# Kernel tuning notes

Measured on AMD Instinct MI355X. Metric: run time of the kernel, lower is better.

Reference implementation:

```python
import jax, jax.numpy as jnp
import numpy as np

B, N, M, H, NH = 128, 4096, 64, 512, 4
IN, OUT = 256, 256
NH2 = 2 * NH  # read/write heads interleaved: even idx = read, odd idx = write
EPS = 1e-8


def setup_inputs() -> dict:
    key = jax.random.key(0)
    ks = jax.random.split(key, 20)
    nrm = lambda k, shape, s=0.05: (jax.random.normal(k, shape, jnp.float32) * s)
    return {
        'in_data': jax.random.normal(ks[0], (B, IN), jnp.float32),
        'memory': jax.random.normal(ks[1], (B, N, M), jnp.float32) * 0.1,
        'h_prev': jax.random.normal(ks[2], (B, H), jnp.float32),
        'c_prev': jax.random.normal(ks[3], (B, H), jnp.float32),
        'prev_reads': jax.random.normal(ks[4], (NH, B, M), jnp.float32),
        'prev_weights': jax.random.uniform(ks[5], (NH2, B, N), jnp.float32),
        # controller LSTMCell (input = in_data ++ prev_reads)
        'W_ih': nrm(ks[6], (4 * H, IN + NH * M)),
        'b_ih': jnp.zeros((4 * H,), jnp.float32),
        'W_hh': nrm(ks[7], (4 * H, H)),
        'b_hh': jnp.zeros((4 * H,), jnp.float32),
        # output layer over [h ++ reads]
        'W_out': nrm(ks[8], (OUT, H + NH * M)),
        'b_out': jnp.zeros((OUT,), jnp.float32),
        # per-head addressing params, stacked over the 2*NH heads (fed with c-state)
        'Wk': nrm(ks[9], (NH2, M, H)), 'bk': jnp.zeros((NH2, M), jnp.float32),
        'Wbeta': nrm(ks[10], (NH2, H)), 'bbeta': jnp.zeros((NH2,), jnp.float32),
        'Wg': nrm(ks[11], (NH2, H)), 'bg': jnp.zeros((NH2,), jnp.float32),
        'Ws': nrm(ks[12], (NH2, 3, H)), 'bs': jnp.zeros((NH2, 3), jnp.float32),
        'Wgam': nrm(ks[13], (NH2, H)), 'bgam': jnp.zeros((NH2,), jnp.float32),
        'We': nrm(ks[14], (NH2, M, H)), 'be': jnp.zeros((NH2, M), jnp.float32),
        'Wa': nrm(ks[15], (NH2, M, H)), 'ba': jnp.zeros((NH2, M), jnp.float32),
    }


def reference(in_data, memory, h_prev, c_prev, prev_reads, prev_weights,
              W_ih, b_ih, W_hh, b_hh, W_out, b_out,
              Wk, bk, Wbeta, bbeta, Wg, bg, Ws, bs, Wgam, bgam, We, be, Wa, ba):
    bsz = in_data.shape[0]
    # controller LSTM step on [x ++ prev_reads]
    x = jnp.concatenate([in_data, jnp.swapaxes(prev_reads, 0, 1).reshape(bsz, -1)], axis=-1)
    gates = x @ W_ih.T + h_prev @ W_hh.T + b_ih + b_hh
    gi, gf, gg, go = jnp.split(gates, 4, axis=-1)
    c = jax.nn.sigmoid(gf) * c_prev + jax.nn.sigmoid(gi) * jnp.tanh(gg)
    h = jax.nn.sigmoid(go) * jnp.tanh(c)  # |h| < 1, so clamp(-20, 20) is identity

    mem = memory
    reads = []
    for i in range(NH2):  # fixed small loop; even = read head, odd = write head
        keyv = c @ Wk[i].T + bk[i]                                    # [B, M]
        beta = jax.nn.softplus(c @ Wbeta[i] + bbeta[i])[:, None]      # [B, 1]
        g = jax.nn.sigmoid(c @ Wg[i] + bg[i])[:, None]                # [B, 1]
        s = jax.nn.softmax(c @ Ws[i].T + bs[i], axis=-1)              # [B, 3]
        gamma = 1.0 + jax.nn.softplus(c @ Wgam[i] + bgam[i])[:, None]  # [B, 1]
        # content addressing: cosine similarity, sharpened softmax
        sim = jnp.einsum('bnm,bm->bn', mem, keyv)
        sim = sim / (jnp.linalg.norm(mem, axis=-1) * jnp.linalg.norm(keyv, axis=-1, keepdims=True) + EPS)
        wc = jax.nn.softmax(beta * sim, axis=-1)
        # interpolate, circular shift (-1, 0, +1), sharpen
        wg_ = g * wc + (1.0 - g) * prev_weights[i]
        wsft = (s[:, 0:1] * jnp.roll(wg_, -1, axis=1)
                + s[:, 1:2] * wg_
                + s[:, 2:3] * jnp.roll(wg_, 1, axis=1))
        wpow = wsft ** gamma
        w = wpow / (jnp.sum(wpow, axis=1, keepdims=True) + EPS)
        if i % 2 == 0:
            reads.append(jnp.einsum('bn,bnm->bm', w, mem))
        else:
            e = jax.nn.sigmoid(c @ We[i].T + be[i])                   # erase [B, M]
            a = jnp.tanh(c @ Wa[i].T + ba[i])                         # add   [B, M]
            mem = mem * (1.0 - w[:, :, None] * e[:, None, :]) + w[:, :, None] * a[:, None, :]

    out = jax.nn.sigmoid(jnp.concatenate([h] + reads, axis=-1) @ W_out.T + b_out)
    return out
```

## Files before the change

kernel.cpp:

```cpp
#include <hip/hip_runtime.h>
#include <math.h>

#define BSZ 128
#define NN_ 4096
#define MM_ 64
#define HH_ 512
#define EPSF 1e-8f

__device__ __forceinline__ float sigmoidf_(float x) { return 1.0f / (1.0f + expf(-x)); }
__device__ __forceinline__ float softplusf_(float x) { return fmaxf(x, 0.0f) + log1pf(expf(-fabsf(x))); }

__global__ __launch_bounds__(256) void k_gemm_gates(const float* __restrict__ in_data,
                                                    const float* __restrict__ prev_reads,
                                                    const float* __restrict__ h_prev,
                                                    const float* __restrict__ W_ih,
                                                    const float* __restrict__ W_hh,
                                                    float* __restrict__ Cp) {
    __shared__ float Alds[64 * 65];
    __shared__ float Wlds[64 * 65];
    int t = threadIdx.x;
    int n0 = blockIdx.x * 64;
    int b0 = blockIdx.y * 64;
    float* C = Cp + (size_t)blockIdx.z * (BSZ * 2048);
    int ob = (t & 15) * 4;
    int bb = (t >> 4) * 4;
    float acc[4][4];
#pragma unroll
    for (int i = 0; i < 4; ++i)
#pragma unroll
        for (int j = 0; j < 4; ++j) acc[i][j] = 0.f;
    for (int kt = 0; kt < 4; ++kt) {
        int k0 = blockIdx.z * 256 + kt * 64;
        __syncthreads();
        for (int i = 0; i < 4; ++i) {
            int f = t + 256 * i;
            int row = f >> 4, kk = (f & 15) * 4;
            int k = k0 + kk;
            float4 v;
            if (k < 256) v = *(const float4*)(in_data + ((b0 + row) << 8) + k);
            else if (k < 512) {
                int q = k - 256;
                v = *(const float4*)(prev_reads + (((q >> 6) * BSZ + b0 + row) << 6) + (q & 63));
            } else v = *(const float4*)(h_prev + ((b0 + row) << 9) + (k - 512));
            Alds[(kk + 0) * 65 + row] = v.x;
            Alds[(kk + 1) * 65 + row] = v.y;
            Alds[(kk + 2) * 65 + row] = v.z;
            Alds[(kk + 3) * 65 + row] = v.w;
        }
        for (int i = 0; i < 4; ++i) {
            int f = t + 256 * i;
            int o = f >> 4, kk = (f & 15) * 4;
            int j = n0 + o, k = k0 + kk;
            const float* src = (k < 512) ? (W_ih + (size_t)j * 512 + k)
                                         : (W_hh + (size_t)j * 512 + (k - 512));
            float4 v = *(const float4*)src;
            Wlds[(kk + 0) * 65 + o] = v.x;
            Wlds[(kk + 1) * 65 + o] = v.y;
            Wlds[(kk + 2) * 65 + o] = v.z;
            Wlds[(kk + 3) * 65 + o] = v.w;
        }
        __syncthreads();
        for (int kk = 0; kk < 64; ++kk) {
            const float* wp = &Wlds[kk * 65 + ob];
            const float* ap = &Alds[kk * 65 + bb];
            float w0 = wp[0], w1 = wp[1], w2 = wp[2], w3 = wp[3];
#pragma unroll
            for (int j = 0; j < 4; ++j) {
                float av = ap[j];
                acc[0][j] = fmaf(w0, av, acc[0][j]);
                acc[1][j] = fmaf(w1, av, acc[1][j]);
                acc[2][j] = fmaf(w2, av, acc[2][j]);
                acc[3][j] = fmaf(w3, av, acc[3][j]);
            }
        }
    }
#pragma unroll
    for (int i = 0; i < 4; ++i)
#pragma unroll
        for (int j = 0; j < 4; ++j)
            C[(size_t)(b0 + bb + j) * 2048 + n0 + ob + i] = acc[i][j];
}

__global__ void k_lstm(const float* __restrict__ gatesP, const float* __restrict__ b_ih,
                       const float* __restrict__ b_hh, const float* __restrict__ c_prev,
                       float* __restrict__ cbuf, float* __restrict__ hbuf) {
    int idx = blockIdx.x * blockDim.x + threadIdx.x;
    if (idx >= BSZ * HH_) return;
    int b = idx >> 9, j = idx & 511;
    float gi = b_ih[j]        + b_hh[j];
    float gf = b_ih[512 + j]  + b_hh[512 + j];
    float gg = b_ih[1024 + j] + b_hh[1024 + j];
    float go = b_ih[1536 + j] + b_hh[1536 + j];
#pragma unroll
    for (int p = 0; p < 4; ++p) {
        const float* gr = gatesP + (size_t)p * (BSZ * 2048) + (size_t)b * 2048;
        gi += gr[j];
        gf += gr[512 + j];
        gg += gr[1024 + j];
        go += gr[1536 + j];
    }
    float cc = sigmoidf_(gf) * c_prev[idx] + sigmoidf_(gi) * tanhf(gg);
    float hh = sigmoidf_(go) * tanhf(cc);
    cbuf[idx] = cc;
    hbuf[idx] = hh;
}

__device__ __forceinline__ const float* whead_row_ptr(const float* Wk, const float* Wbeta,
                                                      const float* Wg, const float* Ws,
                                                      const float* Wgam, const float* We,
                                                      const float* Wa, int r) {
    int i = r / 198, q = r - i * 198;
    if (q < 64)  return Wk + (size_t)((i << 6) + q) * 512;
    if (q == 64) return Wbeta + (size_t)i * 512;
    if (q == 65) return Wg + (size_t)i * 512;
    if (q <= 68) return Ws + (size_t)(i * 3 + q - 66) * 512;
    if (q == 69) return Wgam + (size_t)i * 512;
    if (q < 134) return We + (size_t)((i << 6) + q - 70) * 512;
    return Wa + (size_t)((i << 6) + q - 134) * 512;
}

__global__ __launch_bounds__(256) void k_gemm_head(const float* __restrict__ A,
                                                   const float* __restrict__ Wk,
                                                   const float* __restrict__ Wbeta,
                                                   const float* __restrict__ Wg,
                                                   const float* __restrict__ Ws,
                                                   const float* __restrict__ Wgam,
                                                   const float* __restrict__ We,
                                                   const float* __restrict__ Wa,
                                                   float* __restrict__ Cp) {
    __shared__ float Alds[64 * 65];
    __shared__ float Wlds[64 * 65];
    int t = threadIdx.x;
    int n0 = blockIdx.x * 64;
    int b0 = blockIdx.y * 64;
    float* C = Cp + (size_t)blockIdx.z * (BSZ * 1408);
    int ob = (t & 15) * 4;
    int bb = (t >> 4) * 4;
    float acc[4][4];
#pragma unroll
    for (int i = 0; i < 4; ++i)
#pragma unroll
        for (int j = 0; j < 4; ++j) acc[i][j] = 0.f;
    for (int kt = 0; kt < 4; ++kt) {
        int k0 = blockIdx.z * 256 + kt * 64;
        __syncthreads();
        for (int i = 0; i < 4; ++i) {
            int f = t + 256 * i;
            int row = f >> 4, kk = (f & 15) * 4;
            float4 v = *(const float4*)(A + (size_t)(b0 + row) * 512 + k0 + kk);
            Alds[(kk + 0) * 65 + row] = v.x;
            Alds[(kk + 1) * 65 + row] = v.y;
            Alds[(kk + 2) * 65 + row] = v.z;
            Alds[(kk + 3) * 65 + row] = v.w;
        }
        for (int i = 0; i < 4; ++i) {
            int f = t + 256 * i;
            int o = f >> 4, kk = (f & 15) * 4;
            int r = n0 + o;
            float4 v = make_float4(0.f, 0.f, 0.f, 0.f);
            if (r < 1386) {
                const float* p = whead_row_ptr(Wk, Wbeta, Wg, Ws, Wgam, We, Wa, r) + k0 + kk;
                v = *(const float4*)p;
            }
            Wlds[(kk + 0) * 65 + o] = v.x;
            Wlds[(kk + 1) * 65 + o] = v.y;
            Wlds[(kk + 2) * 65 + o] = v.z;
            Wlds[(kk + 3) * 65 + o] = v.w;
        }
        __syncthreads();
        for (int kk = 0; kk < 64; ++kk) {
            const float* wp = &Wlds[kk * 65 + ob];
            const float* ap = &Alds[kk * 65 + bb];
            float w0 = wp[0], w1 = wp[1], w2 = wp[2], w3 = wp[3];
#pragma unroll
            for (int j = 0; j < 4; ++j) {
                float av = ap[j];
                acc[0][j] = fmaf(w0, av, acc[0][j]);
                acc[1][j] = fmaf(w1, av, acc[1][j]);
                acc[2][j] = fmaf(w2, av, acc[2][j]);
                acc[3][j] = fmaf(w3, av, acc[3][j]);
            }
        }
    }
#pragma unroll
    for (int i = 0; i < 4; ++i)
#pragma unroll
        for (int j = 0; j < 4; ++j)
            C[(size_t)(b0 + bb + j) * 1408 + n0 + ob + i] = acc[i][j];
}

__global__ __launch_bounds__(256) void k_headact(const float* __restrict__ C0,
                                                 const float* __restrict__ C1,
                                                 const float* __restrict__ bk, const float* __restrict__ bbeta,
                                                 const float* __restrict__ bg, const float* __restrict__ bs,
                                                 const float* __restrict__ bgam, const float* __restrict__ be,
                                                 const float* __restrict__ ba,
                                                 float* __restrict__ keys, float* __restrict__ knorm,
                                                 float* __restrict__ betaA, float* __restrict__ gA,
                                                 float* __restrict__ gammaA, float* __restrict__ sA,
                                                 float* __restrict__ eA, float* __restrict__ aA) {
    __shared__ float sk[64];
    __shared__ float s3[3];
    int blk = blockIdx.x;
    int i = blk >> 7, b = blk & 127;
    int q = threadIdx.x;
    float val = 0.f;
    if (q < 198) {
        float bv = (q < 64)   ? bk[(i << 6) + q]
                 : (q == 64)  ? bbeta[i]
                 : (q == 65)  ? bg[i]
                 : (q <= 68)  ? bs[i * 3 + q - 66]
                 : (q == 69)  ? bgam[i]
                 : (q < 134)  ? be[(i << 6) + q - 70]
                              : ba[(i << 6) + q - 134];
        size_t idx = (size_t)b * 1408 + i * 198 + q;
        val = C0[idx] + C1[idx] + bv;
    }
    if (q < 64) { keys[(size_t)(i * BSZ + b) * 64 + q] = val; sk[q] = val * val; }
    if (q >= 66 && q <= 68) s3[q - 66] = val;
    __syncthreads();
    if (q == 0) {
        float s = 0.f;
        for (int m2 = 0; m2 < 64; ++m2) s += sk[m2];
        knorm[i * BSZ + b] = sqrtf(s);
    }
    if (q == 64) betaA[i * BSZ + b] = softplusf_(val);
    if (q == 65) gA[i * BSZ + b] = sigmoidf_(val);
    if (q == 69) gammaA[i * BSZ + b] = 1.f + softplusf_(val);
    if (q == 66) {
        float mx = fmaxf(s3[0], fmaxf(s3[1], s3[2]));
        float e0 = expf(s3[0] - mx), e1 = expf(s3[1] - mx), e2 = expf(s3[2] - mx);
        float inv = 1.f / (e0 + e1 + e2);
        sA[(i * BSZ + b) * 3 + 0] = e0 * inv;
        sA[(i * BSZ + b) * 3 + 1] = e1 * inv;
        sA[(i * BSZ + b) * 3 + 2] = e2 * inv;
    }
    if (q >= 70 && q < 134)  eA[(size_t)(i * BSZ + b) * 64 + (q - 70)] = sigmoidf_(val);
    if (q >= 134 && q < 198) aA[(size_t)(i * BSZ + b) * 64 + (q - 134)] = tanhf(val);
}

__global__ __launch_bounds__(256) void k_pass2(const float* __restrict__ mem,
                                               const float* __restrict__ wbuf,
                                               const float* __restrict__ eA, const float* __restrict__ aA,
                                               const float* __restrict__ keys, const float* __restrict__ knorm,
                                               float* __restrict__ sims, float* __restrict__ r_out,
                                               int napply, int nsims, int sh0, int sh1,
                                               int read_state, int read_head, int read_idx) {
    __shared__ __align__(16) float rbuf[16][64];
    int t = threadIdx.x;
    int lane = t & 15, grp = t >> 4;
    int base = blockIdx.x * 64;
    int b = base >> 12;
    int m4 = lane * 4;
    float4 e1 = *(const float4*)(eA + (size_t)(1 * BSZ + b) * 64 + m4);
    float4 a1 = *(const float4*)(aA + (size_t)(1 * BSZ + b) * 64 + m4);
    float4 e3 = *(const float4*)(eA + (size_t)(3 * BSZ + b) * 64 + m4);
    float4 a3 = *(const float4*)(aA + (size_t)(3 * BSZ + b) * 64 + m4);
    float4 e5 = *(const float4*)(eA + (size_t)(5 * BSZ + b) * 64 + m4);
    float4 a5 = *(const float4*)(aA + (size_t)(5 * BSZ + b) * 64 + m4);
    float4 k0v = make_float4(0.f, 0.f, 0.f, 0.f), k1v = k0v;
    float kn0v = 0.f, kn1v = 0.f;
    if (nsims > 0) { k0v = *(const float4*)(keys + (size_t)(sh0 * BSZ + b) * 64 + m4); kn0v = knorm[sh0 * BSZ + b]; }
    if (nsims > 1) { k1v = *(const float4*)(keys + (size_t)(sh1 * BSZ + b) * 64 + m4); kn1v = knorm[sh1 * BSZ + b]; }
    const float* w1p = wbuf + (size_t)1 * BSZ * NN_;
    const float* w3p = wbuf + (size_t)3 * BSZ * NN_;
    const float* w5p = wbuf + (size_t)5 * BSZ * NN_;
    const float* wrp = (read_head >= 0) ? (wbuf + (size_t)read_head * BSZ * NN_) : nullptr;
    float* sim0 = sims + (size_t)sh0 * BSZ * NN_;
    float* sim1 = sims + (size_t)sh1 * BSZ * NN_;

    float4 racc = make_float4(0.f, 0.f, 0.f, 0.f);
    for (int it = 0; it < 4; ++it) {
        int row = base + it * 16 + grp;
        float4 m = *(const float4*)(mem + (size_t)row * 64 + m4);
        float4 mr = m;
        if (napply >= 1) {
            float w = w1p[row];
            m.x = m.x * (1.f - w * e1.x) + w * a1.x;
            m.y = m.y * (1.f - w * e1.y) + w * a1.y;
            m.z = m.z * (1.f - w * e1.z) + w * a1.z;
            m.w = m.w * (1.f - w * e1.w) + w * a1.w;
            if (read_state == 1) mr = m;
        }
        if (napply >= 2) {
            float w = w3p[row];
            m.x = m.x * (1.f - w * e3.x) + w * a3.x;
            m.y = m.y * (1.f - w * e3.y) + w * a3.y;
            m.z = m.z * (1.f - w * e3.z) + w * a3.z;
            m.w = m.w * (1.f - w * e3.w) + w * a3.w;
            if (read_state == 2) mr = m;
        }
        if (napply >= 3) {
            float w = w5p[row];
            m.x = m.x * (1.f - w * e5.x) + w * a5.x;
            m.y = m.y * (1.f - w * e5.y) + w * a5.y;
            m.z = m.z * (1.f - w * e5.z) + w * a5.z;
            m.w = m.w * (1.f - w * e5.w) + w * a5.w;
            if (read_state == 3) mr = m;
        }
        if (read_head >= 0) {
            float wr = wrp[row];
            racc.x = fmaf(wr, mr.x, racc.x);
            racc.y = fmaf(wr, mr.y, racc.y);
            racc.z = fmaf(wr, mr.z, racc.z);
            racc.w = fmaf(wr, mr.w, racc.w);
        }
        if (nsims > 0) {
            float d0 = m.x * k0v.x + m.y * k0v.y + m.z * k0v.z + m.w * k0v.w;
            float nn = m.x * m.x + m.y * m.y + m.z * m.z + m.w * m.w;
            float d1 = 0.f;
            if (nsims > 1) d1 = m.x * k1v.x + m.y * k1v.y + m.z * k1v.z + m.w * k1v.w;
#pragma unroll
            for (int off = 8; off >= 1; off >>= 1) {
                d0 += __shfl_xor(d0, off, 16);
                nn += __shfl_xor(nn, off, 16);
                if (nsims > 1) d1 += __shfl_xor(d1, off, 16);
            }
            if (lane == 0) {
                float nm = sqrtf(nn);
                sim0[row] = d0 / (nm * kn0v + EPSF);
                if (nsims > 1) sim1[row] = d1 / (nm * kn1v + EPSF);
            }
        }
    }
    if (read_head >= 0) {
        *(float4*)(&rbuf[grp][m4]) = racc;
        __syncthreads();
        if (t < 64) {
            float s = 0.f;
#pragma unroll
            for (int g2 = 0; g2 < 16; ++g2) s += rbuf[g2][t];
            atomicAdd(&r_out[(size_t)(read_idx * BSZ + b) * 64 + t], s);
        }
    }
}

__global__ __launch_bounds__(1024) void k_weights(const float* __restrict__ sims,
                                                  const float* __restrict__ prev_w,
                                                  const float* __restrict__ betaA, const float* __restrict__ gA,
                                                  const float* __restrict__ gammaA, const float* __restrict__ sA,
                                                  float* __restrict__ wout_base, int head0) {
    __shared__ float wg[NN_];
    __shared__ float redm[16], reds[16], redp[16];
    int h = head0 + blockIdx.y, b = blockIdx.x;
    int hb = h * BSZ + b;
    float beta = betaA[hb], g = gA[hb], gamma = gammaA[hb];
    float s0 = sA[hb * 3 + 0], s1 = sA[hb * 3 + 1], s2 = sA[hb * 3 + 2];
    const float* sim = sims + (size_t)hb * NN_;
    const float* pw = prev_w + (size_t)hb * NN_;
    float* wout = wout_base + (size_t)hb * NN_;
    int t = threadIdx.x, wv = t >> 6, ln = t & 63;
    float tv[4];
    float lmax = -3.4e38f;
#pragma unroll
    for (int j = 0; j < 4; ++j) {
        float x = beta * sim[t + 1024 * j];
        tv[j] = x;
        lmax = fmaxf(lmax, x);
    }
#pragma unroll
    for (int off = 32; off >= 1; off >>= 1) lmax = fmaxf(lmax, __shfl_xor(lmax, off));
    if (ln == 0) redm[wv] = lmax;
    __syncthreads();
    float Mx = redm[0];
#pragma unroll
    for (int k = 1; k < 16; ++k) Mx = fmaxf(Mx, redm[k]);
    float lsum = 0.f;
#pragma unroll
    for (int j = 0; j < 4; ++j) { float ex = expf(tv[j] - Mx); tv[j] = ex; lsum += ex; }
#pragma unroll
    for (int off = 32; off >= 1; off >>= 1) lsum += __shfl_xor(lsum, off);
    if (ln == 0) reds[wv] = lsum;
    __syncthreads();
    float S = 0.f;
#pragma unroll
    for (int k = 0; k < 16; ++k) S += reds[k];
    float invS = 1.f / S;
#pragma unroll
    for (int j = 0; j < 4; ++j) {
        int n = t + 1024 * j;
        wg[n] = g * tv[j] * invS + (1.f - g) * pw[n];
    }
    __syncthreads();
    float lsum2 = 0.f;
#pragma unroll
    for (int j = 0; j < 4; ++j) {
        int n = t + 1024 * j;
        float wsft = s0 * wg[(n + 1) & (NN_ - 1)] + s1 * wg[n] + s2 * wg[(n - 1) & (NN_ - 1)];
        float wp = powf(wsft, gamma);
        tv[j] = wp;
        lsum2 += wp;
    }
#pragma unroll
    for (int off = 32; off >= 1; off >>= 1) lsum2 += __shfl_xor(lsum2, off);
    if (ln == 0) redp[wv] = lsum2;
    __syncthreads();
    float S2 = 0.f;
#pragma unroll
    for (int k = 0; k < 16; ++k) S2 += redp[k];
    float inv2 = 1.f / (S2 + EPSF);
#pragma unroll
    for (int j = 0; j < 4; ++j) wout[t + 1024 * j] = tv[j] * inv2;
}

__global__ __launch_bounds__(256) void k_out_full(const float* __restrict__ hbuf,
                                                  const float* __restrict__ rbuf,
                                                  const float* __restrict__ W_out,
                                                  const float* __restrict__ b_out,
                                                  float* __restrict__ out) {
    __shared__ float Alds[64 * 65];
    __shared__ float Wlds[64 * 65];
    int t = threadIdx.x;
    int n0 = blockIdx.x * 64;
    int b0 = blockIdx.y * 64;
    int ob = (t & 15) * 4;
    int bb = (t >> 4) * 4;
    float acc[4][4];
#pragma unroll
    for (int i = 0; i < 4; ++i)
#pragma unroll
        for (int j = 0; j < 4; ++j) acc[i][j] = 0.f;
    for (int k0 = 0; k0 < 768; k0 += 64) {
        __syncthreads();
        for (int i = 0; i < 4; ++i) {
            int f = t + 256 * i;
            int rb = f >> 4, kk = (f & 15) * 4;
            int k = k0 + kk;
            float4 v;
            if (k < 512) v = *(const float4*)(hbuf + ((b0 + rb) << 9) + k);
            else {
                int q = k - 512;
                v = *(const float4*)(rbuf + (((q >> 6) * BSZ + b0 + rb) << 6) + (q & 63));
            }
            Alds[(kk + 0) * 65 + rb] = v.x;
            Alds[(kk + 1) * 65 + rb] = v.y;
            Alds[(kk + 2) * 65 + rb] = v.z;
            Alds[(kk + 3) * 65 + rb] = v.w;
        }
        for (int i = 0; i < 4; ++i) {
            int f = t + 256 * i;
            int o = f >> 4, kk = (f & 15) * 4;
            float4 v = *(const float4*)(W_out + (size_t)(n0 + o) * 768 + k0 + kk);
            Wlds[(kk + 0) * 65 + o] = v.x;
            Wlds[(kk + 1) * 65 + o] = v.y;
            Wlds[(kk + 2) * 65 + o] = v.z;
            Wlds[(kk + 3) * 65 + o] = v.w;
        }
        __syncthreads();
        for (int kk = 0; kk < 64; ++kk) {
            const float* wp = &Wlds[kk * 65 + ob];
            const float* ap = &Alds[kk * 65 + bb];
            float w0 = wp[0], w1 = wp[1], w2 = wp[2], w3 = wp[3];
#pragma unroll
            for (int j = 0; j < 4; ++j) {
                float av = ap[j];
                acc[0][j] = fmaf(w0, av, acc[0][j]);
                acc[1][j] = fmaf(w1, av, acc[1][j]);
                acc[2][j] = fmaf(w2, av, acc[2][j]);
                acc[3][j] = fmaf(w3, av, acc[3][j]);
            }
        }
    }
#pragma unroll
    for (int i = 0; i < 4; ++i)
#pragma unroll
        for (int j = 0; j < 4; ++j)
            out[(size_t)(b0 + bb + j) * 256 + n0 + ob + i] = sigmoidf_(acc[i][j] + b_out[n0 + ob + i]);
}

extern "C" void kernel_launch(void* const* d_in, const int* in_sizes, int n_in,
                              void* d_out, int out_size, void* d_ws, size_t ws_size,
                              hipStream_t stream) {
    const float* in_data      = (const float*)d_in[0];
    const float* memory       = (const float*)d_in[1];
    const float* h_prev       = (const float*)d_in[2];
    const float* c_prev       = (const float*)d_in[3];
    const float* prev_reads   = (const float*)d_in[4];
    const float* prev_weights = (const float*)d_in[5];
    const float* W_ih = (const float*)d_in[6];
    const float* b_ih = (const float*)d_in[7];
    const float* W_hh = (const float*)d_in[8];
    const float* b_hh = (const float*)d_in[9];
    const float* W_out = (const float*)d_in[10];
    const float* b_out = (const float*)d_in[11];
    const float* Wk   = (const float*)d_in[12];
    const float* bk   = (const float*)d_in[13];
    const float* Wbeta = (const float*)d_in[14];
    const float* bbeta = (const float*)d_in[15];
    const float* Wg   = (const float*)d_in[16];
    const float* bg   = (const float*)d_in[17];
    const float* Ws   = (const float*)d_in[18];
    const float* bs   = (const float*)d_in[19];
    const float* Wgam = (const float*)d_in[20];
    const float* bgam = (const float*)d_in[21];
    const float* We   = (const float*)d_in[22];
    const float* be   = (const float*)d_in[23];
    const float* Wa   = (const float*)d_in[24];
    const float* ba   = (const float*)d_in[25];

    float* ws = (float*)d_ws;
    size_t o_r      = 0;
    size_t zero_floats = 32768;
    size_t o_gatesP = zero_floats;
    size_t o_cheadP = o_gatesP + 1048576;
    size_t o_c     = o_cheadP + 360448;
    size_t o_h     = o_c + 65536;
    size_t o_keys  = o_h + 65536;
    size_t o_knorm = o_keys + 57344;
    size_t o_beta  = o_knorm + 1024;
    size_t o_g     = o_beta + 1024;
    size_t o_gamma = o_g + 1024;
    size_t o_s     = o_gamma + 1024;
    size_t o_e     = o_s + 3072;
    size_t o_a     = o_e + 57344;
    size_t o_sims  = o_a + 57344;
    size_t o_w     = o_sims + 3670016;

    float* rbuf   = ws + o_r;
    float* gatesP = ws + o_gatesP;
    float* CheadP = ws + o_cheadP;
    float* cbuf   = ws + o_c;
    float* hbuf   = ws + o_h;
    float* keys   = ws + o_keys;
    float* knorm  = ws + o_knorm;
    float* betaA  = ws + o_beta;
    float* gA     = ws + o_g;
    float* gammaA = ws + o_gamma;
    float* sA     = ws + o_s;
    float* eA     = ws + o_e;
    float* aA     = ws + o_a;
    float* sims   = ws + o_sims;
    float* wbuf   = ws + o_w;

    hipMemsetAsync(d_ws, 0, zero_floats * sizeof(float), stream);

    k_gemm_gates<<<dim3(32, 2, 4), 256, 0, stream>>>(in_data, prev_reads, h_prev, W_ih, W_hh, gatesP);
    k_lstm<<<256, 256, 0, stream>>>(gatesP, b_ih, b_hh, c_prev, cbuf, hbuf);

    k_gemm_head<<<dim3(22, 2, 2), 256, 0, stream>>>(cbuf, Wk, Wbeta, Wg, Ws, Wgam, We, Wa, CheadP);
    k_headact<<<896, 256, 0, stream>>>(CheadP, CheadP + (size_t)BSZ * 1408,
                                       bk, bbeta, bg, bs, bgam, be, ba,
                                       keys, knorm, betaA, gA, gammaA, sA, eA, aA);

    const int PB = BSZ * NN_ / 64;
    k_pass2<<<PB, 256, 0, stream>>>(memory, wbuf, eA, aA, keys, knorm, sims, rbuf,
                                    0, 2, 0, 1, -1, -1, 0);
    k_weights<<<dim3(128, 2), 1024, 0, stream>>>(sims, prev_weights, betaA, gA, gammaA, sA, wbuf, 0);
    k_pass2<<<PB, 256, 0, stream>>>(memory, wbuf, eA, aA, keys, knorm, sims, rbuf,
                                    1, 2, 2, 3, 0, 0, 0);
    k_weights<<<dim3(128, 2), 1024, 0, stream>>>(sims, prev_weights, betaA, gA, gammaA, sA, wbuf, 2);
    k_pass2<<<PB, 256, 0, stream>>>(memory, wbuf, eA, aA, keys, knorm, sims, rbuf,
                                    2, 2, 4, 5, 1, 2, 1);
    k_weights<<<dim3(128, 2), 1024, 0, stream>>>(sims, prev_weights, betaA, gA, gammaA, sA, wbuf, 4);
    k_pass2<<<PB, 256, 0, stream>>>(memory, wbuf, eA, aA, keys, knorm, sims, rbuf,
                                    3, 1, 6, 6, 2, 4, 2);
    k_weights<<<dim3(128, 1), 1024, 0, stream>>>(sims, prev_weights, betaA, gA, gammaA, sA, wbuf, 6);
    k_pass2<<<PB, 256, 0, stream>>>(memory, wbuf, eA, aA, keys, knorm, sims, rbuf,
                                    3, 0, 0, 0, 3, 6, 3);

    k_out_full<<<dim3(4, 2), 256, 0, stream>>>(hbuf, rbuf, W_out, b_out, (float*)d_out);

    (void)in_sizes; (void)n_in; (void)out_size; (void)ws_size;
}
```

Before: 529.8 us.

## Fuse memory passes and weight kernels into one persistent per-batch kernel

```diff
diff --git a/kernel.cpp b/kernel.cpp
--- a/kernel.cpp
+++ b/kernel.cpp
@@ -5,10 +5,18 @@
 #define NN_ 4096
 #define MM_ 64
 #define HH_ 512
+#define HALFN 2048
 #define EPSF 1e-8f
 
 __device__ __forceinline__ float sigmoidf_(float x) { return 1.0f / (1.0f + expf(-x)); }
 __device__ __forceinline__ float softplusf_(float x) { return fmaxf(x, 0.0f) + log1pf(expf(-fabsf(x))); }
+
+__device__ __forceinline__ void agstf(float* p, float v) {
+    __hip_atomic_store(p, v, __ATOMIC_RELAXED, __HIP_MEMORY_SCOPE_AGENT);
+}
+__device__ __forceinline__ float agldf(const float* p) {
+    return __hip_atomic_load(p, __ATOMIC_RELAXED, __HIP_MEMORY_SCOPE_AGENT);
+}
 
 __global__ __launch_bounds__(256) void k_gemm_gates(const float* __restrict__ in_data,
                                                     const float* __restrict__ prev_reads,
@@ -239,168 +247,267 @@
     if (q >= 134 && q < 198) aA[(size_t)(i * BSZ + b) * 64 + (q - 134)] = tanhf(val);
 }
 
-__global__ __launch_bounds__(256) void k_pass2(const float* __restrict__ mem,
-                                               const float* __restrict__ wbuf,
-                                               const float* __restrict__ eA, const float* __restrict__ aA,
-                                               const float* __restrict__ keys, const float* __restrict__ knorm,
-                                               float* __restrict__ sims, float* __restrict__ r_out,
-                                               int napply, int nsims, int sh0, int sh1,
-                                               int read_state, int read_head, int read_idx) {
-    __shared__ __align__(16) float rbuf[16][64];
+__global__ __launch_bounds__(512) void k_mega(const float* __restrict__ mem,
+                                              const float* __restrict__ prev_w,
+                                              const float* __restrict__ eA, const float* __restrict__ aA,
+                                              const float* __restrict__ keys, const float* __restrict__ knorm,
+                                              const float* __restrict__ betaA, const float* __restrict__ gA,
+                                              const float* __restrict__ gammaA, const float* __restrict__ sA,
+                                              float* __restrict__ r_out,
+                                              float* __restrict__ xpay, int* __restrict__ xflag) {
+    __shared__ float w1s[HALFN], w3s[HALFN], w5s[HALFN], wrs[HALFN];
+    __shared__ float sxp[2][HALFN];
+    __shared__ __align__(16) float rred[32][64];
+    __shared__ float xch[8];
+    __shared__ float redu[16];
+
+    int bid = blockIdx.x;
+    int b = bid & 127;
+    int half = bid >> 7;
     int t = threadIdx.x;
     int lane = t & 15, grp = t >> 4;
-    int base = blockIdx.x * 64;
-    int b = base >> 12;
     int m4 = lane * 4;
+    int wv = t >> 6, ln = t & 63;
+    const int n0g = half * HALFN;
+    const int ph = 1 - half;
+
     float4 e1 = *(const float4*)(eA + (size_t)(1 * BSZ + b) * 64 + m4);
     float4 a1 = *(const float4*)(aA + (size_t)(1 * BSZ + b) * 64 + m4);
     float4 e3 = *(const float4*)(eA + (size_t)(3 * BSZ + b) * 64 + m4);
     float4 a3 = *(const float4*)(aA + (size_t)(3 * BSZ + b) * 64 + m4);
     float4 e5 = *(const float4*)(eA + (size_t)(5 * BSZ + b) * 64 + m4);
     float4 a5 = *(const float4*)(aA + (size_t)(5 * BSZ + b) * 64 + m4);
-    float4 k0v = make_float4(0.f, 0.f, 0.f, 0.f), k1v = k0v;
-    float kn0v = 0.f, kn1v = 0.f;
-    if (nsims > 0) { k0v = *(const float4*)(keys + (size_t)(sh0 * BSZ + b) * 64 + m4); kn0v = knorm[sh0 * BSZ + b]; }
-    if (nsims > 1) { k1v = *(const float4*)(keys + (size_t)(sh1 * BSZ + b) * 64 + m4); kn1v = knorm[sh1 * BSZ + b]; }
-    const float* w1p = wbuf + (size_t)1 * BSZ * NN_;
-    const float* w3p = wbuf + (size_t)3 * BSZ * NN_;
-    const float* w5p = wbuf + (size_t)5 * BSZ * NN_;
-    const float* wrp = (read_head >= 0) ? (wbuf + (size_t)read_head * BSZ * NN_) : nullptr;
-    float* sim0 = sims + (size_t)sh0 * BSZ * NN_;
-    float* sim1 = sims + (size_t)sh1 * BSZ * NN_;
-
-    float4 racc = make_float4(0.f, 0.f, 0.f, 0.f);
-    for (int it = 0; it < 4; ++it) {
-        int row = base + it * 16 + grp;
-        float4 m = *(const float4*)(mem + (size_t)row * 64 + m4);
-        float4 mr = m;
-        if (napply >= 1) {
-            float w = w1p[row];
-            m.x = m.x * (1.f - w * e1.x) + w * a1.x;
-            m.y = m.y * (1.f - w * e1.y) + w * a1.y;
-            m.z = m.z * (1.f - w * e1.z) + w * a1.z;
-            m.w = m.w * (1.f - w * e1.w) + w * a1.w;
-            if (read_state == 1) mr = m;
-        }
-        if (napply >= 2) {
-            float w = w3p[row];
-            m.x = m.x * (1.f - w * e3.x) + w * a3.x;
-            m.y = m.y * (1.f - w * e3.y) + w * a3.y;
-            m.z = m.z * (1.f - w * e3.z) + w * a3.z;
-            m.w = m.w * (1.f - w * e3.w) + w * a3.w;
-            if (read_state == 2) mr = m;
-        }
-        if (napply >= 3) {
-            float w = w5p[row];
-            m.x = m.x * (1.f - w * e5.x) + w * a5.x;
-            m.y = m.y * (1.f - w * e5.y) + w * a5.y;
-            m.z = m.z * (1.f - w * e5.z) + w * a5.z;
-            m.w = m.w * (1.f - w * e5.w) + w * a5.w;
-            if (read_state == 3) mr = m;
-        }
-        if (read_head >= 0) {
-            float wr = wrp[row];
-            racc.x = fmaf(wr, mr.x, racc.x);
-            racc.y = fmaf(wr, mr.y, racc.y);
-            racc.z = fmaf(wr, mr.z, racc.z);
-            racc.w = fmaf(wr, mr.w, racc.w);
-        }
+
+    int* myflag = xflag + (b * 2 + half) * 8;
+    int* pflag  = xflag + (b * 2 + ph) * 8;
+    float* mypay = xpay + (size_t)(b * 2 + half) * 64;
+    const float* ppay = xpay + (size_t)(b * 2 + ph) * 64;
+
+    const float* membase = mem + ((size_t)b * 4096 + n0g) * 64;
+
+    const int napplyA[5] = {0, 1, 2, 3, 3};
+    const int nsimsA[5]  = {2, 2, 2, 1, 0};
+    const int rstateA[5] = {-1, 0, 1, 2, 3};
+
+    for (int p = 0; p < 5; ++p) {
+        int napply = napplyA[p], nsims = nsimsA[p], rstate = rstateA[p];
+        bool doread = (p >= 1);
+        float bet0 = 0.f, bet1 = 0.f, kn0 = 0.f, kn1 = 0.f;
+        float4 k0v = make_float4(0.f, 0.f, 0.f, 0.f), k1v = k0v;
         if (nsims > 0) {
-            float d0 = m.x * k0v.x + m.y * k0v.y + m.z * k0v.z + m.w * k0v.w;
-            float nn = m.x * m.x + m.y * m.y + m.z * m.z + m.w * m.w;
-            float d1 = 0.f;
-            if (nsims > 1) d1 = m.x * k1v.x + m.y * k1v.y + m.z * k1v.z + m.w * k1v.w;
-#pragma unroll
-            for (int off = 8; off >= 1; off >>= 1) {
-                d0 += __shfl_xor(d0, off, 16);
-                nn += __shfl_xor(nn, off, 16);
-                if (nsims > 1) d1 += __shfl_xor(d1, off, 16);
-            }
-            if (lane == 0) {
-                float nm = sqrtf(nn);
-                sim0[row] = d0 / (nm * kn0v + EPSF);
-                if (nsims > 1) sim1[row] = d1 / (nm * kn1v + EPSF);
-            }
-        }
-    }
-    if (read_head >= 0) {
-        *(float4*)(&rbuf[grp][m4]) = racc;
-        __syncthreads();
-        if (t < 64) {
-            float s = 0.f;
-#pragma unroll
-            for (int g2 = 0; g2 < 16; ++g2) s += rbuf[g2][t];
-            atomicAdd(&r_out[(size_t)(read_idx * BSZ + b) * 64 + t], s);
-        }
-    }
-}
-
-__global__ __launch_bounds__(1024) void k_weights(const float* __restrict__ sims,
-                                                  const float* __restrict__ prev_w,
-                                                  const float* __restrict__ betaA, const float* __restrict__ gA,
-                                                  const float* __restrict__ gammaA, const float* __restrict__ sA,
-                                                  float* __restrict__ wout_base, int head0) {
-    __shared__ float wg[NN_];
-    __shared__ float redm[16], reds[16], redp[16];
-    int h = head0 + blockIdx.y, b = blockIdx.x;
-    int hb = h * BSZ + b;
-    float beta = betaA[hb], g = gA[hb], gamma = gammaA[hb];
-    float s0 = sA[hb * 3 + 0], s1 = sA[hb * 3 + 1], s2 = sA[hb * 3 + 2];
-    const float* sim = sims + (size_t)hb * NN_;
-    const float* pw = prev_w + (size_t)hb * NN_;
-    float* wout = wout_base + (size_t)hb * NN_;
-    int t = threadIdx.x, wv = t >> 6, ln = t & 63;
-    float tv[4];
-    float lmax = -3.4e38f;
-#pragma unroll
-    for (int j = 0; j < 4; ++j) {
-        float x = beta * sim[t + 1024 * j];
-        tv[j] = x;
-        lmax = fmaxf(lmax, x);
-    }
-#pragma unroll
-    for (int off = 32; off >= 1; off >>= 1) lmax = fmaxf(lmax, __shfl_xor(lmax, off));
-    if (ln == 0) redm[wv] = lmax;
-    __syncthreads();
-    float Mx = redm[0];
-#pragma unroll
-    for (int k = 1; k < 16; ++k) Mx = fmaxf(Mx, redm[k]);
-    float lsum = 0.f;
-#pragma unroll
-    for (int j = 0; j < 4; ++j) { float ex = expf(tv[j] - Mx); tv[j] = ex; lsum += ex; }
-#pragma unroll
-    for (int off = 32; off >= 1; off >>= 1) lsum += __shfl_xor(lsum, off);
-    if (ln == 0) reds[wv] = lsum;
-    __syncthreads();
-    float S = 0.f;
-#pragma unroll
-    for (int k = 0; k < 16; ++k) S += reds[k];
-    float invS = 1.f / S;
-#pragma unroll
-    for (int j = 0; j < 4; ++j) {
-        int n = t + 1024 * j;
-        wg[n] = g * tv[j] * invS + (1.f - g) * pw[n];
-    }
-    __syncthreads();
-    float lsum2 = 0.f;
-#pragma unroll
-    for (int j = 0; j < 4; ++j) {
-        int n = t + 1024 * j;
-        float wsft = s0 * wg[(n + 1) & (NN_ - 1)] + s1 * wg[n] + s2 * wg[(n - 1) & (NN_ - 1)];
-        float wp = powf(wsft, gamma);
-        tv[j] = wp;
-        lsum2 += wp;
-    }
-#pragma unroll
-    for (int off = 32; off >= 1; off >>= 1) lsum2 += __shfl_xor(lsum2, off);
-    if (ln == 0) redp[wv] = lsum2;
-    __syncthreads();
-    float S2 = 0.f;
-#pragma unroll
-    for (int k = 0; k < 16; ++k) S2 += redp[k];
-    float inv2 = 1.f / (S2 + EPSF);
-#pragma unroll
-    for (int j = 0; j < 4; ++j) wout[t + 1024 * j] = tv[j] * inv2;
+            int hh = 2 * p;
+            bet0 = betaA[hh * BSZ + b];
+            k0v = *(const float4*)(keys + (size_t)(hh * BSZ + b) * 64 + m4);
+            kn0 = knorm[hh * BSZ + b];
+        }
+        if (nsims > 1) {
+            int hh = 2 * p + 1;
+            bet1 = betaA[hh * BSZ + b];
+            k1v = *(const float4*)(keys + (size_t)(hh * BSZ + b) * 64 + m4);
+            kn1 = knorm[hh * BSZ + b];
+        }
+        float4 racc = make_float4(0.f, 0.f, 0.f, 0.f);
+        for (int rc = 0; rc < 64; ++rc) {
+            int nl = rc * 32 + grp;
+            float4 m = *(const float4*)(membase + (size_t)nl * 64 + m4);
+            float4 mr = m;
+            if (napply >= 1) {
+                float w = w1s[nl];
+                m.x = m.x * (1.f - w * e1.x) + w * a1.x;
+                m.y = m.y * (1.f - w * e1.y) + w * a1.y;
+                m.z = m.z * (1.f - w * e1.z) + w * a1.z;
+                m.w = m.w * (1.f - w * e1.w) + w * a1.w;
+                if (rstate == 1) mr = m;
+            }
+            if (napply >= 2) {
+                float w = w3s[nl];
+                m.x = m.x * (1.f - w * e3.x) + w * a3.x;
+                m.y = m.y * (1.f - w * e3.y) + w * a3.y;
+                m.z = m.z * (1.f - w * e3.z) + w * a3.z;
+                m.w = m.w * (1.f - w * e3.w) + w * a3.w;
+                if (rstate == 2) mr = m;
+            }
+            if (napply >= 3) {
+                float w = w5s[nl];
+                m.x = m.x * (1.f - w * e5.x) + w * a5.x;
+                m.y = m.y * (1.f - w * e5.y) + w * a5.y;
+                m.z = m.z * (1.f - w * e5.z) + w * a5.z;
+                m.w = m.w * (1.f - w * e5.w) + w * a5.w;
+                if (rstate == 3) mr = m;
+            }
+            if (doread) {
+                float wr = wrs[nl];
+                racc.x = fmaf(wr, mr.x, racc.x);
+                racc.y = fmaf(wr, mr.y, racc.y);
+                racc.z = fmaf(wr, mr.z, racc.z);
+                racc.w = fmaf(wr, mr.w, racc.w);
+            }
+            if (nsims > 0) {
+                float d0 = m.x * k0v.x + m.y * k0v.y + m.z * k0v.z + m.w * k0v.w;
+                float nn = m.x * m.x + m.y * m.y + m.z * m.z + m.w * m.w;
+                float d1 = 0.f;
+                if (nsims > 1) d1 = m.x * k1v.x + m.y * k1v.y + m.z * k1v.z + m.w * k1v.w;
+#pragma unroll
+                for (int off = 8; off >= 1; off >>= 1) {
+                    d0 += __shfl_xor(d0, off, 16);
+                    nn += __shfl_xor(nn, off, 16);
+                    if (nsims > 1) d1 += __shfl_xor(d1, off, 16);
+                }
+                if (lane == 0) {
+                    float nm = sqrtf(nn);
+                    sxp[0][nl] = expf(bet0 * (d0 / (nm * kn0 + EPSF)));
+                    if (nsims > 1) sxp[1][nl] = expf(bet1 * (d1 / (nm * kn1 + EPSF)));
+                }
+            }
+        }
+        if (doread) {
+            *(float4*)(&rred[grp][m4]) = racc;
+            __syncthreads();
+            if (t < 64) {
+                float s = 0.f;
+#pragma unroll
+                for (int g2 = 0; g2 < 32; ++g2) s += rred[g2][t];
+                atomicAdd(&r_out[(size_t)((p - 1) * BSZ + b) * 64 + t], s);
+            }
+        }
+        __syncthreads();
+        if (p == 4) break;
+
+        int h0 = 2 * p, h1 = 2 * p + 1;
+        int nheads = (p < 3) ? 2 : 1;
+        int se = 2 * p, so = 2 * p + 1;
+        float p0 = 0.f, p1 = 0.f;
+#pragma unroll
+        for (int j = 0; j < 4; ++j) {
+            int n = t + 512 * j;
+            p0 += sxp[0][n];
+            if (nheads > 1) p1 += sxp[1][n];
+        }
+#pragma unroll
+        for (int off = 32; off >= 1; off >>= 1) {
+            p0 += __shfl_xor(p0, off);
+            p1 += __shfl_xor(p1, off);
+        }
+        if (ln == 0) { redu[wv] = p0; redu[8 + wv] = p1; }
+        __syncthreads();
+        if (t == 0) {
+            float P0 = 0.f, P1 = 0.f;
+#pragma unroll
+            for (int w = 0; w < 8; ++w) { P0 += redu[w]; P1 += redu[8 + w]; }
+            float* mp = mypay + se * 8;
+            agstf(mp + 0, P0);
+            agstf(mp + 1, sxp[0][0]);
+            agstf(mp + 2, sxp[0][HALFN - 1]);
+            agstf(mp + 3, P1);
+            agstf(mp + 4, (nheads > 1) ? sxp[1][0] : 0.f);
+            agstf(mp + 5, (nheads > 1) ? sxp[1][HALFN - 1] : 0.f);
+            __hip_atomic_store(&myflag[se], 1, __ATOMIC_RELEASE, __HIP_MEMORY_SCOPE_AGENT);
+            int spins = 0;
+            while (__hip_atomic_load(&pflag[se], __ATOMIC_ACQUIRE, __HIP_MEMORY_SCOPE_AGENT) == 0) {
+                __builtin_amdgcn_s_sleep(2);
+                if (++spins > (1 << 26)) break;
+            }
+            const float* pp = ppay + se * 8;
+            float q0 = agldf(pp + 0), ef0 = agldf(pp + 1), el0 = agldf(pp + 2);
+            float q1 = agldf(pp + 3), ef1 = agldf(pp + 4), el1 = agldf(pp + 5);
+            float invS0 = 1.f / (P0 + q0);
+            float invS1 = (nheads > 1) ? 1.f / (P1 + q1) : 0.f;
+            float g0v = gA[h0 * BSZ + b];
+            size_t base0 = (size_t)(h0 * BSZ + b) * 4096;
+            xch[0] = invS0;
+            xch[1] = invS1;
+            xch[2] = g0v * el0 * invS0 + (1.f - g0v) * prev_w[base0 + ph * HALFN + HALFN - 1];
+            xch[3] = g0v * ef0 * invS0 + (1.f - g0v) * prev_w[base0 + ph * HALFN];
+            if (nheads > 1) {
+                float g1v = gA[h1 * BSZ + b];
+                size_t base1 = (size_t)(h1 * BSZ + b) * 4096;
+                xch[4] = g1v * el1 * invS1 + (1.f - g1v) * prev_w[base1 + ph * HALFN + HALFN - 1];
+                xch[5] = g1v * ef1 * invS1 + (1.f - g1v) * prev_w[base1 + ph * HALFN];
+            }
+        }
+        __syncthreads();
+        float invS0 = xch[0], invS1 = xch[1];
+        float bL0 = xch[2], bR0 = xch[3], bL1 = xch[4], bR1 = xch[5];
+        float g0v = gA[h0 * BSZ + b], gam0 = gammaA[h0 * BSZ + b];
+        float s00 = sA[(h0 * BSZ + b) * 3 + 0], s01 = sA[(h0 * BSZ + b) * 3 + 1], s02 = sA[(h0 * BSZ + b) * 3 + 2];
+        const float* pw0 = prev_w + (size_t)(h0 * BSZ + b) * 4096 + n0g;
+#pragma unroll
+        for (int j = 0; j < 4; ++j) {
+            int n = t + 512 * j;
+            sxp[0][n] = g0v * sxp[0][n] * invS0 + (1.f - g0v) * pw0[n];
+        }
+        __syncthreads();
+        float tv0[4];
+        float lp0 = 0.f;
+#pragma unroll
+        for (int j = 0; j < 4; ++j) {
+            int n = t + 512 * j;
+            float left = (n == 0) ? bL0 : sxp[0][n - 1];
+            float right = (n == HALFN - 1) ? bR0 : sxp[0][n + 1];
+            float wsft = s00 * right + s01 * sxp[0][n] + s02 * left;
+            float wp = powf(wsft, gam0);
+            tv0[j] = wp;
+            lp0 += wp;
+        }
+        float tv1[4] = {0.f, 0.f, 0.f, 0.f};
+        float lp1 = 0.f;
+        if (nheads > 1) {
+            float g1v = gA[h1 * BSZ + b], gam1 = gammaA[h1 * BSZ + b];
+            float s10 = sA[(h1 * BSZ + b) * 3 + 0], s11 = sA[(h1 * BSZ + b) * 3 + 1], s12 = sA[(h1 * BSZ + b) * 3 + 2];
+            const float* pw1 = prev_w + (size_t)(h1 * BSZ + b) * 4096 + n0g;
+#pragma unroll
+            for (int j = 0; j < 4; ++j) {
+                int n = t + 512 * j;
+                sxp[1][n] = g1v * sxp[1][n] * invS1 + (1.f - g1v) * pw1[n];
+            }
+            __syncthreads();
+#pragma unroll
+            for (int j = 0; j < 4; ++j) {
+                int n = t + 512 * j;
+                float left = (n == 0) ? bL1 : sxp[1][n - 1];
+                float right = (n == HALFN - 1) ? bR1 : sxp[1][n + 1];
+                float wsft = s10 * right + s11 * sxp[1][n] + s12 * left;
+                float wp = powf(wsft, gam1);
+                tv1[j] = wp;
+                lp1 += wp;
+            }
+        }
+#pragma unroll
+        for (int off = 32; off >= 1; off >>= 1) {
+            lp0 += __shfl_xor(lp0, off);
+            lp1 += __shfl_xor(lp1, off);
+        }
+        if (ln == 0) { redu[wv] = lp0; redu[8 + wv] = lp1; }
+        __syncthreads();
+        if (t == 0) {
+            float S0 = 0.f, S1 = 0.f;
+#pragma unroll
+            for (int w = 0; w < 8; ++w) { S0 += redu[w]; S1 += redu[8 + w]; }
+            float* mp = mypay + so * 8;
+            agstf(mp + 0, S0);
+            agstf(mp + 1, S1);
+            __hip_atomic_store(&myflag[so], 1, __ATOMIC_RELEASE, __HIP_MEMORY_SCOPE_AGENT);
+            int spins = 0;
+            while (__hip_atomic_load(&pflag[so], __ATOMIC_ACQUIRE, __HIP_MEMORY_SCOPE_AGENT) == 0) {
+                __builtin_amdgcn_s_sleep(2);
+                if (++spins > (1 << 26)) break;
+            }
+            float r0 = agldf(ppay + so * 8 + 0);
+            float r1 = agldf(ppay + so * 8 + 1);
+            xch[0] = 1.f / (S0 + r0 + EPSF);
+            xch[1] = (nheads > 1) ? 1.f / (S1 + r1 + EPSF) : 0.f;
+        }
+        __syncthreads();
+        float inv20 = xch[0], inv21 = xch[1];
+        float* slot1 = (p == 0) ? w1s : (p == 1) ? w3s : w5s;
+#pragma unroll
+        for (int j = 0; j < 4; ++j) {
+            int n = t + 512 * j;
+            wrs[n] = tv0[j] * inv20;
+            if (nheads > 1) slot1[n] = tv1[j] * inv21;
+        }
+        __syncthreads();
+    }
 }
 
 __global__ __launch_bounds__(256) void k_out_full(const float* __restrict__ hbuf,
@@ -500,23 +607,25 @@
 
     float* ws = (float*)d_ws;
     size_t o_r      = 0;
-    size_t zero_floats = 32768;
-    size_t o_gatesP = zero_floats;
+    size_t o_flag   = 32768;
+    size_t zero_floats = o_flag + 2048;
+    size_t o_xpay   = zero_floats;
+    size_t o_gatesP = o_xpay + 16384;
     size_t o_cheadP = o_gatesP + 1048576;
-    size_t o_c     = o_cheadP + 360448;
-    size_t o_h     = o_c + 65536;
-    size_t o_keys  = o_h + 65536;
-    size_t o_knorm = o_keys + 57344;
-    size_t o_beta  = o_knorm + 1024;
-    size_t o_g     = o_beta + 1024;
-    size_t o_gamma = o_g + 1024;
-    size_t o_s     = o_gamma + 1024;
-    size_t o_e     = o_s + 3072;
-    size_t o_a     = o_e + 57344;
-    size_t o_sims  = o_a + 57344;
-    size_t o_w     = o_sims + 3670016;
+    size_t o_c      = o_cheadP + 360448;
+    size_t o_h      = o_c + 65536;
+    size_t o_keys   = o_h + 65536;
+    size_t o_knorm  = o_keys + 57344;
+    size_t o_beta   = o_knorm + 1024;
+    size_t o_g      = o_beta + 1024;
+    size_t o_gamma  = o_g + 1024;
+    size_t o_s      = o_gamma + 1024;
+    size_t o_e      = o_s + 3072;
+    size_t o_a      = o_e + 57344;
 
     float* rbuf   = ws + o_r;
+    int*   xflag  = (int*)(ws + o_flag);
+    float* xpay   = ws + o_xpay;
     float* gatesP = ws + o_gatesP;
     float* CheadP = ws + o_cheadP;
     float* cbuf   = ws + o_c;
@@ -529,8 +638,6 @@
     float* sA     = ws + o_s;
     float* eA     = ws + o_e;
     float* aA     = ws + o_a;
-    float* sims   = ws + o_sims;
-    float* wbuf   = ws + o_w;
 
     hipMemsetAsync(d_ws, 0, zero_floats * sizeof(float), stream);
 
@@ -542,21 +649,8 @@
                                        bk, bbeta, bg, bs, bgam, be, ba,
                                        keys, knorm, betaA, gA, gammaA, sA, eA, aA);
 
-    const int PB = BSZ * NN_ / 64;
-    k_pass2<<<PB, 256, 0, stream>>>(memory, wbuf, eA, aA, keys, knorm, sims, rbuf,
-                                    0, 2, 0, 1, -1, -1, 0);
-    k_weights<<<dim3(128, 2), 1024, 0, stream>>>(sims, prev_weights, betaA, gA, gammaA, sA, wbuf, 0);
-    k_pass2<<<PB, 256, 0, stream>>>(memory, wbuf, eA, aA, keys, knorm, sims, rbuf,
-                                    1, 2, 2, 3, 0, 0, 0);
-    k_weights<<<dim3(128, 2), 1024, 0, stream>>>(sims, prev_weights, betaA, gA, gammaA, sA, wbuf, 2);
-    k_pass2<<<PB, 256, 0, stream>>>(memory, wbuf, eA, aA, keys, knorm, sims, rbuf,
-                                    2, 2, 4, 5, 1, 2, 1);
-    k_weights<<<dim3(128, 2), 1024, 0, stream>>>(sims, prev_weights, betaA, gA, gammaA, sA, wbuf, 4);
-    k_pass2<<<PB, 256, 0, stream>>>(memory, wbuf, eA, aA, keys, knorm, sims, rbuf,
-                                    3, 1, 6, 6, 2, 4, 2);
-    k_weights<<<dim3(128, 1), 1024, 0, stream>>>(sims, prev_weights, betaA, gA, gammaA, sA, wbuf, 6);
-    k_pass2<<<PB, 256, 0, stream>>>(memory, wbuf, eA, aA, keys, knorm, sims, rbuf,
-                                    3, 0, 0, 0, 3, 6, 3);
+    k_mega<<<256, 512, 0, stream>>>(memory, prev_weights, eA, aA, keys, knorm,
+                                    betaA, gA, gammaA, sA, rbuf, xpay, xflag);
 
     k_out_full<<<dim3(4, 2), 256, 0, stream>>>(hbuf, rbuf, W_out, b_out, (float*)d_out);
 
```

Result: slower. 635.4 us (+19.9%).
